# Kernel tuning notes

Measured on AMD Instinct MI355X. Metric: run time of the kernel, lower is better.

Reference implementation:

```python
import jax, jax.numpy as jnp
import numpy as np

N, E, D_IN, D_HID, D_OUT = 100000, 1600000, 128, 128, 40

def _sage_pool(x, src, dst, Wp, bp, Ws, Wn, b, n_nodes):
    # DGL SAGEConv 'pool': h_pool = relu(fc_pool(x)); h_neigh = max over in-neighbors;
    # out = fc_self(x) + fc_neigh(h_neigh) + bias
    hp = jax.nn.relu(x @ Wp + bp)                       # [N, d]
    msg = hp[src]                                        # [E, d] gather
    agg = jax.ops.segment_max(msg, dst, num_segments=n_nodes)  # [N, d] scatter-max
    agg = jnp.where(jnp.isfinite(agg), agg, 0.0)         # zero-in-degree nodes -> 0
    return x @ Ws + agg @ Wn + b

def setup_inputs() -> dict:
    key = jax.random.key(0)
    ks = jax.random.split(key, 14)
    def lin(k, i, o):
        return jax.random.normal(k, (i, o), dtype=jnp.float32) / np.sqrt(i)
    return {
        "in_feat": jax.random.normal(ks[0], (N, D_IN), dtype=jnp.float32),
        "src": jax.random.randint(ks[1], (E,), 0, N),
        "dst": jax.random.randint(ks[2], (E,), 0, N),
        "Wp1": lin(ks[3], D_IN, D_IN), "bp1": jnp.zeros((D_IN,), jnp.float32),
        "Ws1": lin(ks[4], D_IN, D_HID), "Wn1": lin(ks[5], D_IN, D_HID),
        "b1": jnp.zeros((D_HID,), jnp.float32),
        "Wp2": lin(ks[6], D_HID, D_HID), "bp2": jnp.zeros((D_HID,), jnp.float32),
        "Ws2": lin(ks[7], D_HID, D_OUT), "Wn2": lin(ks[8], D_HID, D_OUT),
        "b2": jnp.zeros((D_OUT,), jnp.float32),
    }

def reference(in_feat, src, dst, Wp1, bp1, Ws1, Wn1, b1, Wp2, bp2, Ws2, Wn2, b2):
    h = _sage_pool(in_feat, src, dst, Wp1, bp1, Ws1, Wn1, b1, N)
    h = jax.nn.relu(h)
    # dropout is identity at inference (eval mode)
    return _sage_pool(h, src, dst, Wp2, bp2, Ws2, Wn2, b2, N)
```

## Files before the change

kernel.cpp:

```cpp
#include <hip/hip_runtime.h>
#include <stdint.h>

#define NN 100000
#define NE 1600000
#define NB 391

using u16 = unsigned short;
using u32 = unsigned int;

typedef __attribute__((ext_vector_type(8))) short bf16x8;
typedef __attribute__((ext_vector_type(4))) float f32x4;

__device__ inline u16 f2b(float f){
  u32 u = __float_as_uint(f);
  u32 r = (u + 0x7fffu + ((u >> 16) & 1u)) >> 16;
  return (u16)r;
}

__device__ inline bf16x8 cvt8(const float* __restrict__ p){
  float4 a = *(const float4*)p;
  float4 b = *(const float4*)(p + 4);
  union { u32 w[4]; bf16x8 v; } u;
  u.w[0] = (u32)f2b(a.x) | ((u32)f2b(a.y) << 16);
  u.w[1] = (u32)f2b(a.z) | ((u32)f2b(a.w) << 16);
  u.w[2] = (u32)f2b(b.x) | ((u32)f2b(b.y) << 16);
  u.w[3] = (u32)f2b(b.z) | ((u32)f2b(b.w) << 16);
  return u.v;
}

__global__ void k_prep(const float* __restrict__ Wp1, const float* __restrict__ Ws1,
                       const float* __restrict__ Wn1, const float* __restrict__ Wp2,
                       const float* __restrict__ Ws2, const float* __restrict__ Wn2,
                       u16* __restrict__ wpT1, u16* __restrict__ wc1T,
                       u16* __restrict__ wpT2, u16* __restrict__ wc2T,
                       int* __restrict__ cb){
  int i = blockIdx.x * 256 + threadIdx.x;
  if (i < NB) cb[i] = 0;
  if (i < 16384){ int n = i >> 7, k = i & 127;
    wpT1[n*128 + k] = f2b(Wp1[k*128 + n]);
    wpT2[n*128 + k] = f2b(Wp2[k*128 + n]);
  }
  if (i < 32768){ int n = i >> 8, k = i & 255;
    float v = (k < 128) ? Ws1[k*128 + n] : Wn1[(k-128)*128 + n];
    wc1T[n*256 + k] = f2b(v);
  }
  if (i < 12288){ int n = i >> 8, k = i & 255;
    float v = 0.f;
    if (n < 40) v = (k < 128) ? Ws2[k*40 + n] : Wn2[(k-128)*40 + n];
    wc2T[n*256 + k] = f2b(v);
  }
}

__global__ __launch_bounds__(512) void k_cb_hist(const int* __restrict__ dst,
                                                 int* __restrict__ cb){
  __shared__ int h[NB];
  for (int i = threadIdx.x; i < NB; i += 512) h[i] = 0;
  __syncthreads();
  int e0 = blockIdx.x * 2048 + threadIdx.x;
  #pragma unroll
  for (int j = 0; j < 4; j++){
    int e = e0 + j * 512;
    if (e < NE) atomicAdd(&h[dst[e] >> 8], 1);
  }
  __syncthreads();
  for (int i = threadIdx.x; i < NB; i += 512)
    if (h[i]) atomicAdd(&cb[i], h[i]);
}

__global__ __launch_bounds__(512) void k_cb_scan(const int* __restrict__ cb,
                                                 int* __restrict__ cbo,
                                                 int* __restrict__ curB){
  __shared__ int s[512];
  int tid = threadIdx.x;
  int v = (tid < NB) ? cb[tid] : 0;
  s[tid] = v;
  __syncthreads();
  #pragma unroll
  for (int off = 1; off < 512; off <<= 1){
    int t = (tid >= off) ? s[tid - off] : 0;
    __syncthreads();
    s[tid] += t;
    __syncthreads();
  }
  int ex = s[tid] - v;
  if (tid < NB){ cbo[tid] = ex; curB[tid] = ex; }
  if (tid == 511) cbo[NB] = s[511];
}

__global__ __launch_bounds__(1024) void k_part(const int* __restrict__ src,
                                               const int* __restrict__ dst,
                                               int* __restrict__ curB,
                                               u32* __restrict__ part){
  __shared__ int hist[NB], scn[NB], cur[NB], base[NB];
  __shared__ int2 stage[4096];
  const int tid = threadIdx.x;
  const int e0 = blockIdx.x * 4096;
  const int cnt = min(4096, NE - e0);
  for (int i = tid; i < NB; i += 1024) hist[i] = 0;
  __syncthreads();
  int2 ed[4];
  #pragma unroll
  for (int j = 0; j < 4; j++){
    int e = e0 + j * 1024 + tid;
    if (e < NE){
      ed[j].x = src[e]; ed[j].y = dst[e];
      atomicAdd(&hist[ed[j].y >> 8], 1);
    }
  }
  __syncthreads();
  int hv = (tid < NB) ? hist[tid] : 0;
  if (tid < NB) base[tid] = hv ? atomicAdd(&curB[tid], hv) : 0;
  #pragma unroll
  for (int off = 1; off < 512; off <<= 1){
    int t = 0;
    if (tid < 512 && tid >= off && tid - off < NB) t = hist[tid - off];
    __syncthreads();
    if (tid < NB) hist[tid] += t;
    __syncthreads();
  }
  if (tid < NB){ int ex = hist[tid] - hv; scn[tid] = ex; cur[tid] = ex; }
  __syncthreads();
  #pragma unroll
  for (int j = 0; j < 4; j++){
    int e = e0 + j * 1024 + tid;
    if (e < NE){
      int slot = atomicAdd(&cur[ed[j].y >> 8], 1);
      stage[slot] = ed[j];
    }
  }
  __syncthreads();
  for (int i = tid; i < cnt; i += 1024){
    int2 p = stage[i];
    int b = p.y >> 8;
    part[base[b] + (i - scn[b])] = ((u32)(p.y & 255) << 17) | (u32)p.x;
  }
}

__global__ __launch_bounds__(256) void k_bsort(const u32* __restrict__ part,
                                               const int* __restrict__ cbo,
                                               int* __restrict__ rp,
                                               int* __restrict__ esrc){
  __shared__ int cnt[256], sc[256], cur[256];
  const int tid = threadIdx.x;
  const int b = blockIdx.x;
  const int lo = cbo[b], hi = cbo[b + 1];
  cnt[tid] = 0;
  __syncthreads();
  for (int i = lo + tid; i < hi; i += 256)
    atomicAdd(&cnt[part[i] >> 17], 1);
  __syncthreads();
  sc[tid] = cnt[tid];
  __syncthreads();
  #pragma unroll
  for (int off = 1; off < 256; off <<= 1){
    int t = (tid >= off) ? sc[tid - off] : 0;
    __syncthreads();
    sc[tid] += t;
    __syncthreads();
  }
  int ex = sc[tid] - cnt[tid];
  int n = (b << 8) + tid;
  if (n < NN) rp[n] = lo + ex;
  if (b == NB - 1 && tid == 0) rp[NN] = hi;
  cur[tid] = lo + ex;
  __syncthreads();
  for (int i = lo + tid; i < hi; i += 256){
    u32 p = part[i];
    int pos = atomicAdd(&cur[p >> 17], 1);
    esrc[pos] = (int)(p & 0x1FFFFu);
  }
}

__global__ void k_agg(const u16* __restrict__ hp, const int* __restrict__ rp,
                      const int* __restrict__ esrc, u16* __restrict__ agg){
  int node = blockIdx.x * 4 + (threadIdx.x >> 6);
  if (node >= NN) return;
  const int lane = threadIdx.x & 63;
  const int half = lane >> 5;
  const int l32  = lane & 31;
  const int lo = rp[node], hi = rp[node + 1];
  u32 m0 = 0, m1 = 0;
  for (int i = lo; i < hi; i += 16){
    int s[8];
    #pragma unroll
    for (int j = 0; j < 8; j++){
      int ii = i + 2 * j + half; if (ii >= hi) ii = hi - 1;
      s[j] = esrc[ii];
    }
    uint2 v[8];
    #pragma unroll
    for (int j = 0; j < 8; j++)
      v[j] = *(const uint2*)&hp[(size_t)s[j] * 128 + l32 * 4];
    #pragma unroll
    for (int j = 0; j < 8; j++){
      asm("v_pk_max_u16 %0, %0, %1" : "+v"(m0) : "v"(v[j].x));
      asm("v_pk_max_u16 %0, %0, %1" : "+v"(m1) : "v"(v[j].y));
    }
  }
  u32 t0 = (u32)__shfl_xor((int)m0, 32);
  u32 t1 = (u32)__shfl_xor((int)m1, 32);
  asm("v_pk_max_u16 %0, %0, %1" : "+v"(m0) : "v"(t0));
  asm("v_pk_max_u16 %0, %0, %1" : "+v"(m1) : "v"(t1));
  if (half == 0)
    *(uint2*)&agg[(size_t)node * 128 + l32 * 4] = make_uint2(m0, m1);
}

template<int K, int NOUT, int NOUTR, bool A1F32, bool HASA2, bool RELU, bool OUTF32>
__global__ __launch_bounds__(512)
void k_dgemm(const void* __restrict__ A1p, const u16* __restrict__ A2,
             const u16* __restrict__ Wt, const float* __restrict__ bias,
             void* __restrict__ outp)
{
  constexpr int KP  = K + 8;
  constexpr int NTI = NOUT / 16;
  __shared__ u16 W_lds[NOUT * KP];
  const int tid  = threadIdx.x;
  const int row0 = blockIdx.x * 128;
  const int wave = tid >> 6, lane = tid & 63;
  const int colb = lane & 15;
  const int koff = (lane >> 4) * 8;

  for (int c = tid; c < NOUT * (K / 8); c += 512){
    int n = c / (K / 8), kc = c % (K / 8);
    *(uint4*)&W_lds[n * KP + kc * 8] = *(const uint4*)&Wt[n * K + kc * 8];
  }
  __syncthreads();

  const int rowl = wave * 16 + colb;
  const int rA   = min(row0 + rowl, NN - 1);

  f32x4 acc[NTI] = {};

  #pragma unroll
  for (int k0 = 0; k0 < K; k0 += 64){
    bf16x8 af0, af1;
    if (A1F32 && k0 < 128){
      const float* A = (const float*)A1p;
      af0 = cvt8(&A[(size_t)rA * 128 + k0 + koff]);
      af1 = cvt8(&A[(size_t)rA * 128 + k0 + 32 + koff]);
    } else {
      const u16* A = (HASA2 && k0 >= 128) ? A2 : (const u16*)A1p;
      int kb = (HASA2 && k0 >= 128) ? (k0 - 128) : k0;
      af0 = *(const bf16x8*)&A[(size_t)rA * 128 + kb + koff];
      af1 = *(const bf16x8*)&A[(size_t)rA * 128 + kb + 32 + koff];
    }
    #pragma unroll
    for (int nt = 0; nt < NTI; nt++){
      const u16* Wr = &W_lds[(nt * 16 + colb) * KP + k0];
      bf16x8 b0 = *(const bf16x8*)&Wr[koff];
      bf16x8 b1 = *(const bf16x8*)&Wr[32 + koff];
      acc[nt] = __builtin_amdgcn_mfma_f32_16x16x32_bf16(af0, b0, acc[nt], 0, 0, 0);
      acc[nt] = __builtin_amdgcn_mfma_f32_16x16x32_bf16(af1, b1, acc[nt], 0, 0, 0);
    }
  }

  const int rowc = wave * 16 + ((lane >> 4) << 2);
  #pragma unroll
  for (int nt = 0; nt < NTI; nt++){
    int col = nt * 16 + colb;
    if (col >= NOUTR) continue;
    float bv = bias[col];
    #pragma unroll
    for (int r = 0; r < 4; r++){
      int gr = row0 + rowc + r;
      if (gr >= NN) continue;
      float v = acc[nt][r] + bv;
      if (RELU) v = fmaxf(v, 0.f);
      if (OUTF32) ((float*)outp)[(size_t)gr * NOUTR + col] = v;
      else        ((u16*)outp)[(size_t)gr * NOUTR + col] = f2b(v);
    }
  }
}

extern "C" void kernel_launch(void* const* d_in, const int* in_sizes, int n_in,
                              void* d_out, int out_size, void* d_ws, size_t ws_size,
                              hipStream_t stream){
  const float* x   = (const float*)d_in[0];
  const int*   src = (const int*)d_in[1];
  const int*   dst = (const int*)d_in[2];
  const float* Wp1 = (const float*)d_in[3];
  const float* bp1 = (const float*)d_in[4];
  const float* Ws1 = (const float*)d_in[5];
  const float* Wn1 = (const float*)d_in[6];
  const float* b1  = (const float*)d_in[7];
  const float* Wp2 = (const float*)d_in[8];
  const float* bp2 = (const float*)d_in[9];
  const float* Ws2 = (const float*)d_in[10];
  const float* Wn2 = (const float*)d_in[11];
  const float* b2  = (const float*)d_in[12];

  char* ws = (char*)d_ws;
  u16* wpT1 = (u16*)(ws + 0);
  u16* wc1T = (u16*)(ws + 32768);
  u16* wpT2 = (u16*)(ws + 98304);
  u16* wc2T = (u16*)(ws + 131072);
  int* cb   = (int*)(ws + 155648);
  int* cbo  = (int*)(ws + 157696);
  int* curB = (int*)(ws + 159744);
  int* rp   = (int*)(ws + 161792);
  u32* part = (u32*)(ws + 561920);
  u16* h    = (u16*)(ws + 561920);
  int* esrc = (int*)(ws + 26161920);
  u16* hp   = (u16*)(ws + 32561920);
  u16* agg  = (u16*)(ws + 58161920);

  k_prep<<<128, 256, 0, stream>>>(Wp1, Ws1, Wn1, Wp2, Ws2, Wn2,
                                  wpT1, wc1T, wpT2, wc2T, cb);
  k_cb_hist<<<(NE + 2047) / 2048, 512, 0, stream>>>(dst, cb);
  k_cb_scan<<<1, 512, 0, stream>>>(cb, cbo, curB);
  k_part<<<(NE + 4095) / 4096, 1024, 0, stream>>>(src, dst, curB, part);
  k_bsort<<<NB, 256, 0, stream>>>(part, cbo, rp, esrc);

  k_dgemm<128,128,128, true ,false,true ,false>
      <<<(NN + 127) / 128, 512, 0, stream>>>(x, nullptr, wpT1, bp1, hp);
  k_agg<<<(NN + 3) / 4, 256, 0, stream>>>(hp, rp, esrc, agg);
  k_dgemm<256,128,128, true ,true ,true ,false>
      <<<(NN + 127) / 128, 512, 0, stream>>>(x, agg, wc1T, b1, h);
  k_dgemm<128,128,128, false,false,true ,false>
      <<<(NN + 127) / 128, 512, 0, stream>>>(h, nullptr, wpT2, bp2, hp);
  k_agg<<<(NN + 3) / 4, 256, 0, stream>>>(hp, rp, esrc, agg);
  k_dgemm<256, 48, 40, false,true ,false,true >
      <<<(NN + 127) / 128, 512, 0, stream>>>(h, agg, wc2T, b2, d_out);
}
```

Measured before the change: 251.0 us.

## Fuse CSR build stages and overlap first pool GEMM with edge partitioning

Merges the weight-prep and bucket-histogram kernels, removes the standalone scan kernel by redoing the bucket prefix scan inside each partition and bucket-sort block, and runs the first-layer pool GEMM in the same launch as the edge partition, with separate block ranges for each. The aim is to cut kernel launch count and serialisation and to fill the GPU with both kinds of work at once. In exchange, every block now repeats a redundant 512-element scan, and a memset is added to zero the bucket counters.

```diff
diff --git a/kernel.cpp b/kernel.cpp
--- a/kernel.cpp
+++ b/kernel.cpp
@@ -3,7 +3,9 @@
 
 #define NN 100000
 #define NE 1600000
-#define NB 391
+#define NBK 391
+#define NPOOL 782
+#define NPART 782
 
 using u16 = unsigned short;
 using u32 = unsigned int;
@@ -28,14 +30,24 @@
   return u.v;
 }
 
-__global__ void k_prep(const float* __restrict__ Wp1, const float* __restrict__ Ws1,
-                       const float* __restrict__ Wn1, const float* __restrict__ Wp2,
-                       const float* __restrict__ Ws2, const float* __restrict__ Wn2,
-                       u16* __restrict__ wpT1, u16* __restrict__ wc1T,
-                       u16* __restrict__ wpT2, u16* __restrict__ wc2T,
-                       int* __restrict__ cb){
-  int i = blockIdx.x * 256 + threadIdx.x;
-  if (i < NB) cb[i] = 0;
+__global__ __launch_bounds__(512)
+void k_prep(const float* __restrict__ Wp1, const float* __restrict__ Ws1,
+            const float* __restrict__ Wn1, const float* __restrict__ Wp2,
+            const float* __restrict__ Ws2, const float* __restrict__ Wn2,
+            u16* __restrict__ wpT1, u16* __restrict__ wc1T,
+            u16* __restrict__ wpT2, u16* __restrict__ wc2T,
+            const int* __restrict__ dst, int* __restrict__ cb){
+  __shared__ int hcb[NBK];
+  const int tid = threadIdx.x;
+  for (int i = tid; i < NBK; i += 512) hcb[i] = 0;
+  __syncthreads();
+  int e0 = blockIdx.x * 2048 + tid;
+  #pragma unroll
+  for (int j = 0; j < 4; j++){
+    int e = e0 + j * 512;
+    if (e < NE) atomicAdd(&hcb[dst[e] >> 8], 1);
+  }
+  int i = blockIdx.x * 512 + tid;
   if (i < 16384){ int n = i >> 7, k = i & 127;
     wpT1[n*128 + k] = f2b(Wp1[k*128 + n]);
     wpT2[n*128 + k] = f2b(Wp2[k*128 + n]);
@@ -49,122 +61,164 @@
     if (n < 40) v = (k < 128) ? Ws2[k*40 + n] : Wn2[(k-128)*40 + n];
     wc2T[n*256 + k] = f2b(v);
   }
-}
-
-__global__ __launch_bounds__(512) void k_cb_hist(const int* __restrict__ dst,
-                                                 int* __restrict__ cb){
-  __shared__ int h[NB];
-  for (int i = threadIdx.x; i < NB; i += 512) h[i] = 0;
-  __syncthreads();
-  int e0 = blockIdx.x * 2048 + threadIdx.x;
-  #pragma unroll
-  for (int j = 0; j < 4; j++){
-    int e = e0 + j * 512;
-    if (e < NE) atomicAdd(&h[dst[e] >> 8], 1);
-  }
-  __syncthreads();
-  for (int i = threadIdx.x; i < NB; i += 512)
-    if (h[i]) atomicAdd(&cb[i], h[i]);
-}
-
-__global__ __launch_bounds__(512) void k_cb_scan(const int* __restrict__ cb,
-                                                 int* __restrict__ cbo,
-                                                 int* __restrict__ curB){
-  __shared__ int s[512];
-  int tid = threadIdx.x;
-  int v = (tid < NB) ? cb[tid] : 0;
-  s[tid] = v;
-  __syncthreads();
-  #pragma unroll
-  for (int off = 1; off < 512; off <<= 1){
-    int t = (tid >= off) ? s[tid - off] : 0;
-    __syncthreads();
-    s[tid] += t;
-    __syncthreads();
-  }
-  int ex = s[tid] - v;
-  if (tid < NB){ cbo[tid] = ex; curB[tid] = ex; }
-  if (tid == 511) cbo[NB] = s[511];
-}
-
-__global__ __launch_bounds__(1024) void k_part(const int* __restrict__ src,
-                                               const int* __restrict__ dst,
-                                               int* __restrict__ curB,
-                                               u32* __restrict__ part){
-  __shared__ int hist[NB], scn[NB], cur[NB], base[NB];
-  __shared__ int2 stage[4096];
+  __syncthreads();
+  for (int i2 = tid; i2 < NBK; i2 += 512)
+    if (hcb[i2]) atomicAdd(&cb[i2], hcb[i2]);
+}
+
+__global__ __launch_bounds__(512)
+void k_pp(const float* __restrict__ x, const u16* __restrict__ wpT1,
+          const float* __restrict__ bp1, u16* __restrict__ hp,
+          const int* __restrict__ src, const int* __restrict__ dst,
+          const int* __restrict__ cb, int* __restrict__ curB,
+          u32* __restrict__ part){
+  __shared__ __align__(16) char smem[34816];
   const int tid = threadIdx.x;
-  const int e0 = blockIdx.x * 4096;
-  const int cnt = min(4096, NE - e0);
-  for (int i = tid; i < NB; i += 1024) hist[i] = 0;
-  __syncthreads();
-  int2 ed[4];
-  #pragma unroll
-  for (int j = 0; j < 4; j++){
-    int e = e0 + j * 1024 + tid;
-    if (e < NE){
-      ed[j].x = src[e]; ed[j].y = dst[e];
-      atomicAdd(&hist[ed[j].y >> 8], 1);
-    }
-  }
-  __syncthreads();
-  int hv = (tid < NB) ? hist[tid] : 0;
-  if (tid < NB) base[tid] = hv ? atomicAdd(&curB[tid], hv) : 0;
-  #pragma unroll
-  for (int off = 1; off < 512; off <<= 1){
-    int t = 0;
-    if (tid < 512 && tid >= off && tid - off < NB) t = hist[tid - off];
-    __syncthreads();
-    if (tid < NB) hist[tid] += t;
-    __syncthreads();
-  }
-  if (tid < NB){ int ex = hist[tid] - hv; scn[tid] = ex; cur[tid] = ex; }
-  __syncthreads();
-  #pragma unroll
-  for (int j = 0; j < 4; j++){
-    int e = e0 + j * 1024 + tid;
-    if (e < NE){
-      int slot = atomicAdd(&cur[ed[j].y >> 8], 1);
-      stage[slot] = ed[j];
-    }
-  }
-  __syncthreads();
-  for (int i = tid; i < cnt; i += 1024){
-    int2 p = stage[i];
-    int b = p.y >> 8;
-    part[base[b] + (i - scn[b])] = ((u32)(p.y & 255) << 17) | (u32)p.x;
-  }
-}
-
-__global__ __launch_bounds__(256) void k_bsort(const u32* __restrict__ part,
-                                               const int* __restrict__ cbo,
+  if (blockIdx.x < NPOOL){
+    u16* W_lds = (u16*)smem;
+    const int row0 = blockIdx.x * 128;
+    const int wave = tid >> 6, lane = tid & 63;
+    const int colb = lane & 15;
+    const int koff = (lane >> 4) * 8;
+    for (int c = tid; c < 128 * 16; c += 512){
+      int n = c >> 4, kc = c & 15;
+      *(uint4*)&W_lds[n * 136 + kc * 8] = *(const uint4*)&wpT1[n * 128 + kc * 8];
+    }
+    __syncthreads();
+    const int rA = min(row0 + wave * 16 + colb, NN - 1);
+    f32x4 acc[8] = {};
+    #pragma unroll
+    for (int k0 = 0; k0 < 128; k0 += 64){
+      bf16x8 af0 = cvt8(&x[(size_t)rA * 128 + k0 + koff]);
+      bf16x8 af1 = cvt8(&x[(size_t)rA * 128 + k0 + 32 + koff]);
+      #pragma unroll
+      for (int nt = 0; nt < 8; nt++){
+        const u16* Wr = &W_lds[(nt * 16 + colb) * 136 + k0];
+        bf16x8 b0 = *(const bf16x8*)&Wr[koff];
+        bf16x8 b1 = *(const bf16x8*)&Wr[32 + koff];
+        acc[nt] = __builtin_amdgcn_mfma_f32_16x16x32_bf16(af0, b0, acc[nt], 0, 0, 0);
+        acc[nt] = __builtin_amdgcn_mfma_f32_16x16x32_bf16(af1, b1, acc[nt], 0, 0, 0);
+      }
+    }
+    const int rowc = wave * 16 + ((lane >> 4) << 2);
+    #pragma unroll
+    for (int nt = 0; nt < 8; nt++){
+      int col = nt * 16 + colb;
+      float bv = bp1[col];
+      #pragma unroll
+      for (int r = 0; r < 4; r++){
+        int gr = row0 + rowc + r;
+        if (gr < NN)
+          hp[(size_t)gr * 128 + col] = f2b(fmaxf(acc[nt][r] + bv, 0.f));
+      }
+    }
+  } else {
+    int* hist = (int*)smem;
+    int* scn  = hist + NBK;
+    int* cur  = scn  + NBK;
+    int* base = cur  + NBK;
+    int2* stage = (int2*)(base + NBK);
+    int* s512 = (int*)stage;
+    const int e0 = (blockIdx.x - NPOOL) * 2048;
+    const int cnt = min(2048, NE - e0);
+    for (int i = tid; i < NBK; i += 512) hist[i] = 0;
+    __syncthreads();
+    int2 ed[4];
+    #pragma unroll
+    for (int j = 0; j < 4; j++){
+      int e = e0 + j * 512 + tid;
+      if (e < NE){
+        ed[j].x = src[e]; ed[j].y = dst[e];
+        atomicAdd(&hist[ed[j].y >> 8], 1);
+      }
+    }
+    __syncthreads();
+    int cv = (tid < NBK) ? cb[tid] : 0;
+    s512[tid] = cv;
+    __syncthreads();
+    #pragma unroll
+    for (int off = 1; off < 512; off <<= 1){
+      int t = (tid >= off) ? s512[tid - off] : 0;
+      __syncthreads();
+      s512[tid] += t;
+      __syncthreads();
+    }
+    int gex = s512[tid] - cv;
+    int hv = (tid < NBK) ? hist[tid] : 0;
+    if (tid < NBK) base[tid] = gex + (hv ? atomicAdd(&curB[tid], hv) : 0);
+    __syncthreads();
+    s512[tid] = hv;
+    __syncthreads();
+    #pragma unroll
+    for (int off = 1; off < 512; off <<= 1){
+      int t = (tid >= off) ? s512[tid - off] : 0;
+      __syncthreads();
+      s512[tid] += t;
+      __syncthreads();
+    }
+    if (tid < NBK){ int ex = s512[tid] - hv; scn[tid] = ex; cur[tid] = ex; }
+    __syncthreads();
+    #pragma unroll
+    for (int j = 0; j < 4; j++){
+      int e = e0 + j * 512 + tid;
+      if (e < NE){
+        int slot = atomicAdd(&cur[ed[j].y >> 8], 1);
+        stage[slot] = ed[j];
+      }
+    }
+    __syncthreads();
+    for (int i = tid; i < cnt; i += 512){
+      int2 p = stage[i];
+      int b = p.y >> 8;
+      part[base[b] + (i - scn[b])] = ((u32)(p.y & 255) << 17) | (u32)p.x;
+    }
+  }
+}
+
+__global__ __launch_bounds__(512) void k_bsort(const u32* __restrict__ part,
+                                               const int* __restrict__ cb,
                                                int* __restrict__ rp,
                                                int* __restrict__ esrc){
+  __shared__ int s512[512];
   __shared__ int cnt[256], sc[256], cur[256];
+  __shared__ int lohi[2];
   const int tid = threadIdx.x;
   const int b = blockIdx.x;
-  const int lo = cbo[b], hi = cbo[b + 1];
-  cnt[tid] = 0;
-  __syncthreads();
-  for (int i = lo + tid; i < hi; i += 256)
+  int cv = (tid < NBK) ? cb[tid] : 0;
+  s512[tid] = cv;
+  __syncthreads();
+  #pragma unroll
+  for (int off = 1; off < 512; off <<= 1){
+    int t = (tid >= off) ? s512[tid - off] : 0;
+    __syncthreads();
+    s512[tid] += t;
+    __syncthreads();
+  }
+  if (tid == b){ lohi[0] = s512[tid] - cv; lohi[1] = s512[tid]; }
+  if (tid < 256) cnt[tid] = 0;
+  __syncthreads();
+  const int lo = lohi[0], hi = lohi[1];
+  for (int i = lo + tid; i < hi; i += 512)
     atomicAdd(&cnt[part[i] >> 17], 1);
   __syncthreads();
-  sc[tid] = cnt[tid];
+  if (tid < 256) sc[tid] = cnt[tid];
   __syncthreads();
   #pragma unroll
   for (int off = 1; off < 256; off <<= 1){
-    int t = (tid >= off) ? sc[tid - off] : 0;
-    __syncthreads();
-    sc[tid] += t;
-    __syncthreads();
-  }
-  int ex = sc[tid] - cnt[tid];
-  int n = (b << 8) + tid;
-  if (n < NN) rp[n] = lo + ex;
-  if (b == NB - 1 && tid == 0) rp[NN] = hi;
-  cur[tid] = lo + ex;
-  __syncthreads();
-  for (int i = lo + tid; i < hi; i += 256){
+    int t = (tid < 256 && tid >= off) ? sc[tid - off] : 0;
+    __syncthreads();
+    if (tid < 256) sc[tid] += t;
+    __syncthreads();
+  }
+  if (tid < 256){
+    int ex = sc[tid] - cnt[tid];
+    int n = (b << 8) + tid;
+    if (n < NN) rp[n] = lo + ex;
+    cur[tid] = lo + ex;
+  }
+  if (b == NBK - 1 && tid == 0) rp[NN] = hi;
+  __syncthreads();
+  for (int i = lo + tid; i < hi; i += 512){
     u32 p = part[i];
     int pos = atomicAdd(&cur[p >> 17], 1);
     esrc[pos] = (int)(p & 0x1FFFFu);
@@ -226,9 +280,7 @@
   }
   __syncthreads();
 
-  const int rowl = wave * 16 + colb;
-  const int rA   = min(row0 + rowl, NN - 1);
-
+  const int rA = min(row0 + wave * 16 + colb, NN - 1);
   f32x4 acc[NTI] = {};
 
   #pragma unroll
@@ -295,8 +347,7 @@
   u16* wpT2 = (u16*)(ws + 98304);
   u16* wc2T = (u16*)(ws + 131072);
   int* cb   = (int*)(ws + 155648);
-  int* cbo  = (int*)(ws + 157696);
-  int* curB = (int*)(ws + 159744);
+  int* curB = (int*)(ws + 157696);
   int* rp   = (int*)(ws + 161792);
   u32* part = (u32*)(ws + 561920);
   u16* h    = (u16*)(ws + 561920);
@@ -304,15 +355,12 @@
   u16* hp   = (u16*)(ws + 32561920);
   u16* agg  = (u16*)(ws + 58161920);
 
-  k_prep<<<128, 256, 0, stream>>>(Wp1, Ws1, Wn1, Wp2, Ws2, Wn2,
-                                  wpT1, wc1T, wpT2, wc2T, cb);
-  k_cb_hist<<<(NE + 2047) / 2048, 512, 0, stream>>>(dst, cb);
-  k_cb_scan<<<1, 512, 0, stream>>>(cb, cbo, curB);
-  k_part<<<(NE + 4095) / 4096, 1024, 0, stream>>>(src, dst, curB, part);
-  k_bsort<<<NB, 256, 0, stream>>>(part, cbo, rp, esrc);
-
-  k_dgemm<128,128,128, true ,false,true ,false>
-      <<<(NN + 127) / 128, 512, 0, stream>>>(x, nullptr, wpT1, bp1, hp);
+  hipMemsetAsync(ws + 155648, 0, 4096, stream);
+  k_prep<<<(NE + 2047) / 2048, 512, 0, stream>>>(Wp1, Ws1, Wn1, Wp2, Ws2, Wn2,
+                                                 wpT1, wc1T, wpT2, wc2T, dst, cb);
+  k_pp<<<NPOOL + NPART, 512, 0, stream>>>(x, wpT1, bp1, hp, src, dst, cb, curB, part);
+  k_bsort<<<NBK, 512, 0, stream>>>(part, cb, rp, esrc);
+
   k_agg<<<(NN + 3) / 4, 256, 0, stream>>>(hp, rp, esrc, agg);
   k_dgemm<256,128,128, true ,true ,true ,false>
       <<<(NN + 127) / 128, 512, 0, stream>>>(x, agg, wc1T, b1, h);
```

Result: faster. 244.0 us (median of 2 runs) (-2.8%).
